# Kernel tuning notes

Hardware: AMD Instinct MI355X
Metric: run time of the kernel (lower is better)

The kernel has to match this reference:

```python
import jax, jax.numpy as jnp
import numpy as np

D_MODEL = 128
NUM_HEADS = 4
D_HEAD = 32
ATTN_COEFF = 0.5
BATCH = 2
SEQ = 4096


def setup_inputs() -> dict:
    key = jax.random.key(0)
    k1, k2, k3, k4, k5 = jax.random.split(key, 5)
    std = 1.0 / np.sqrt(D_MODEL)
    x = jax.random.normal(k1, (BATCH, SEQ, D_MODEL), dtype=jnp.float32)
    W_K = jax.random.normal(k2, (NUM_HEADS, D_HEAD, D_MODEL), dtype=jnp.float32) * std
    W_Q = jax.random.normal(k3, (NUM_HEADS, D_HEAD, D_MODEL), dtype=jnp.float32) * std
    W_V = jax.random.normal(k4, (NUM_HEADS, D_HEAD, D_MODEL), dtype=jnp.float32) * std
    W_O = jax.random.normal(k5, (D_MODEL, NUM_HEADS * D_HEAD), dtype=jnp.float32) * std
    return {"x": x, "W_K": W_K, "W_Q": W_Q, "W_V": W_V, "W_O": W_O}


def reference(x, W_K, W_Q, W_V, W_O):
    batch, seq, _ = x.shape
    # projections: [B, H, S, Dh]
    k = jnp.einsum('ihd,bpd->biph', W_K, x)
    q = jnp.einsum('ihd,bpd->biph', W_Q, x)
    v = jnp.einsum('ihd,bpd->biph', W_V, x)
    # scores: [B, H, Sq, Sk]
    scores = jnp.einsum('biph,biqh->biqp', k, q) / np.sqrt(D_HEAD).astype(np.float32)
    # NOTE: original code builds a causal mask but never applies it; faithful omission.
    attn = jax.nn.softmax(scores, axis=-1)
    # post-softmax affine blend with uniform offset
    attn = attn * ATTN_COEFF + (1.0 - ATTN_COEFF)
    z = jnp.einsum('biph,biqp->biqh', v, attn)          # [B, H, S, Dh]
    z_flat = jnp.transpose(z, (0, 2, 1, 3)).reshape(batch, seq, NUM_HEADS * D_HEAD)
    out = jnp.einsum('df,bpf->bpd', W_O, z_flat)        # [B, S, D]
    return out
```

## Files before the change

### kernel.cpp

```cpp
#include <hip/hip_runtime.h>

#define SQ 4096
#define NB 2
#define NH 4
#define DH 32
#define DM 128

typedef float f32x16 __attribute__((ext_vector_type(16)));
typedef float f32x4  __attribute__((ext_vector_type(4)));
typedef __bf16 bf16x8 __attribute__((ext_vector_type(8)));
typedef unsigned int uint4v __attribute__((ext_vector_type(4)));
typedef unsigned short u16;

#define AS1 __attribute__((address_space(1)))
#define AS3 __attribute__((address_space(3)))

union B8 { uint4v u; bf16x8 b; };

__device__ inline u16 f2bf(float x) {
  unsigned u = __builtin_bit_cast(unsigned, x);
  unsigned r = (u + 0x7FFF + ((u >> 16) & 1)) >> 16;
  return (u16)r;
}

__device__ inline unsigned cvt_pk_bf16(float a, float b) {
  unsigned r;
  asm("v_cvt_pk_bf16_f32 %0, %1, %2" : "=v"(r) : "v"(a), "v"(b));
  return r;
}

__device__ inline void swap32(unsigned &a, unsigned &b) {
  asm("v_permlane32_swap_b32 %0, %1" : "+v"(a), "+v"(b));
}

#if __has_builtin(__builtin_amdgcn_exp2f)
#define EX2 __builtin_amdgcn_exp2f
#else
#define EX2 exp2f
#endif

__device__ inline float xhalf_add(float x) {
  unsigned ua = __builtin_bit_cast(unsigned, x), ub = ua;
  asm("v_permlane32_swap_b32 %0, %1" : "+v"(ua), "+v"(ub));
  return __builtin_bit_cast(float, ua) + __builtin_bit_cast(float, ub);
}

__device__ inline void gload16(const void* g, void* l) {
  __builtin_amdgcn_global_load_lds((const AS1 void*)g, (AS3 void*)l, 16, 0, 0);
}

__device__ inline bf16x8 ld_cvt8(const float* p) {
  f32x4 a = *(const f32x4*)p;
  f32x4 b = *(const f32x4*)(p + 4);
  B8 r;
  r.u[0] = cvt_pk_bf16(a[0], a[1]);
  r.u[1] = cvt_pk_bf16(a[2], a[3]);
  r.u[2] = cvt_pk_bf16(b[0], b[1]);
  r.u[3] = cvt_pk_bf16(b[2], b[3]);
  return r.b;
}

__global__ __launch_bounds__(256) void kprep(const float* __restrict__ x,
                                             const float* __restrict__ Wo,
                                             u16* __restrict__ wob,
                                             float* __restrict__ xsum) {
  const int bid = blockIdx.x, t = threadIdx.x;
  if (bid < 256) {
    const int b = bid >> 7, rblk = bid & 127;
    const int d = t & 127, rh = t >> 7;
    const float* xp = x + ((size_t)b * SQ + rblk * 32) * DM + d;
    float a = 0.f;
    for (int r = rh; r < 32; r += 2) a += xp[(size_t)r * DM];
    __shared__ float red[2][DM];
    red[rh][d] = a;
    __syncthreads();
    if (t < DM) atomicAdd(&xsum[b * DM + t], red[0][t] + red[1][t]);
  } else {
    for (int i = t; i < DM * DM; i += 256) wob[i] = f2bf(Wo[i]);
  }
}

__global__ __launch_bounds__(256) void kprojc(const float* __restrict__ x,
                                              const float* __restrict__ Wk,
                                              const float* __restrict__ Wq,
                                              const float* __restrict__ Wv,
                                              const float* __restrict__ Wo,
                                              const float* __restrict__ xsum,
                                              u16* __restrict__ qb,
                                              u16* __restrict__ kb,
                                              u16* __restrict__ vt,
                                              float* __restrict__ cvec) {
  const int by = blockIdx.y;
  const int t = threadIdx.x;
  if (by == 12) {
    if (blockIdx.x >= NB) return;
    const int b = blockIdx.x;
    __shared__ float xs[DM], vs[DM];
    if (t < DM) xs[t] = xsum[b * DM + t];
    __syncthreads();
    const int c = t >> 1, half = t & 1;
    float a = 0.f;
    const float* wr = Wv + c * DM + half * 64;
    const float* xh = xs + half * 64;
    for (int i = 0; i < 64; ++i) a += wr[i] * xh[i];
    a += __shfl_xor(a, 1, 64);
    if (half == 0) vs[c] = a;
    __syncthreads();
    float a2 = 0.f;
    const float* wr2 = Wo + c * DM + half * 64;
    const float* vh = vs + half * 64;
    for (int i = 0; i < 64; ++i) a2 += wr2[i] * vh[i];
    a2 += __shfl_xor(a2, 1, 64);
    if (half == 0) cvec[b * DM + c] = 0.5f * a2;
    return;
  }
  const int lane = t & 63, wid = t >> 6;
  const int l31 = lane & 31, hi = lane >> 5;
  const int mat = by >> 2, h = by & 3;
  const int p0 = (blockIdx.x * 4 + wid) * 32;
  const float* xrow = x + (size_t)(p0 + l31) * DM + 8 * hi;
  const float* W = (mat == 0) ? Wk : (mat == 1 ? Wq : Wv);
  const float* wrow = W + (h * 32 + l31) * DM + 8 * hi;
  f32x16 acc;
#pragma unroll
  for (int r = 0; r < 16; ++r) acc[r] = 0.f;
#pragma unroll
  for (int ks = 0; ks < 8; ++ks) {
    bf16x8 af = ld_cvt8(xrow + ks * 16);
    bf16x8 wf = ld_cvt8(wrow + ks * 16);
    acc = __builtin_amdgcn_mfma_f32_32x32x16_bf16(af, wf, acc, 0, 0, 0);
  }
  const float QS = 1.4426950408889634f / 5.656854249492380f;
  const int b = p0 >> 12, pl = p0 & (SQ - 1);
  const size_t bh = (size_t)b * NH + h;
  if (mat == 0) {
    u16* dst = kb + (bh * SQ + pl) * DH + l31;
#pragma unroll
    for (int r = 0; r < 16; ++r) {
      int row = (r & 3) + 8 * (r >> 2) + 4 * hi;
      dst[(size_t)row * DH] = f2bf(acc[r]);
    }
  } else if (mat == 1) {
    u16* dst = qb + (bh * SQ + pl) * DH + l31;
#pragma unroll
    for (int r = 0; r < 16; ++r) {
      int row = (r & 3) + 8 * (r >> 2) + 4 * hi;
      dst[(size_t)row * DH] = f2bf(acc[r] * QS);
    }
  } else {
    u16* dst = vt + ((bh * (SQ / 32) + (pl >> 5)) * DH + l31) * 32;
#pragma unroll
    for (int r = 0; r < 16; ++r) {
      int row = (r & 3) + 8 * (r >> 2) + 4 * hi;
      dst[row] = f2bf(acc[r]);
    }
  }
}

#define STAGE(T, B) {                                              \
  const char* kg_ = kgbase + (size_t)(T) * 8192;                   \
  const char* vg_ = vgbase + (size_t)(T) * 8192;                   \
  gload16(kg_,        &klds[B][woff]);                             \
  gload16(kg_ + 1024, &klds[B][woff + 1024]);                      \
  gload16(vg_,        &vlds[B][woff]);                             \
  gload16(vg_ + 1024, &vlds[B][woff + 1024]);                      \
}

#define SUB(S) {                                                                   \
  const int off_ = (S)*2048 + lbase;                                               \
  B8 k0_, k1_;                                                                     \
  k0_.u = *(const uint4v*)(kl + off_ + kx0);                                       \
  k1_.u = *(const uint4v*)(kl + off_ + kx1);                                       \
  __builtin_amdgcn_s_setprio(1);                                                   \
  f32x16 sc = __builtin_amdgcn_mfma_f32_32x32x16_bf16(k0_.b, qf0.b, zacc, 0,0,0);  \
  sc = __builtin_amdgcn_mfma_f32_32x32x16_bf16(k1_.b, qf1.b, sc, 0, 0, 0);         \
  __builtin_amdgcn_s_setprio(0);                                                   \
  float p_[16];                                                                    \
  _Pragma("unroll") for (int r = 0; r < 16; ++r) p_[r] = EX2(sc[r]);               \
  float ls = ((p_[0]+p_[1])+(p_[2]+p_[3]))+((p_[4]+p_[5])+(p_[6]+p_[7]));          \
  ls += ((p_[8]+p_[9])+(p_[10]+p_[11]))+((p_[12]+p_[13])+(p_[14]+p_[15]));         \
  s += ls;                                                                         \
  unsigned w0 = cvt_pk_bf16(p_[0], p_[1]),  w1 = cvt_pk_bf16(p_[2], p_[3]);        \
  unsigned w2 = cvt_pk_bf16(p_[4], p_[5]),  w3 = cvt_pk_bf16(p_[6], p_[7]);        \
  unsigned w4 = cvt_pk_bf16(p_[8], p_[9]),  w5 = cvt_pk_bf16(p_[10], p_[11]);      \
  unsigned w6 = cvt_pk_bf16(p_[12], p_[13]), w7 = cvt_pk_bf16(p_[14], p_[15]);     \
  swap32(w0, w2); swap32(w1, w3); swap32(w4, w6); swap32(w5, w7);                  \
  B8 bp0_, bp1_;                                                                   \
  bp0_.u[0] = w0; bp0_.u[1] = w1; bp0_.u[2] = w2; bp0_.u[3] = w3;                  \
  bp1_.u[0] = w4; bp1_.u[1] = w5; bp1_.u[2] = w6; bp1_.u[3] = w7;                  \
  B8 v0_, v1_;                                                                     \
  v0_.u = *(const uint4v*)(vl + off_ + kx0);                                       \
  v1_.u = *(const uint4v*)(vl + off_ + kx1);                                       \
  __builtin_amdgcn_s_setprio(1);                                                   \
  acc = __builtin_amdgcn_mfma_f32_32x32x16_bf16(v0_.b, bp0_.b, acc, 0, 0, 0);      \
  acc = __builtin_amdgcn_mfma_f32_32x32x16_bf16(v1_.b, bp1_.b, acc, 0, 0, 0);      \
  __builtin_amdgcn_s_setprio(0);                                                   \
}

__global__ __launch_bounds__(256) void kattn(const u16* __restrict__ qb,
                                             const u16* __restrict__ kb,
                                             const u16* __restrict__ vt,
                                             u16* __restrict__ yb) {
  __shared__ char klds[2][8192];
  __shared__ char vlds[2][8192];
  const int t = threadIdx.x, lane = t & 63, wid = t >> 6;
  const int l31 = lane & 31, hi = lane >> 5;
  const int bh = blockIdx.x & 7;
  const int qbase = (blockIdx.x >> 3) * 128 + wid * 32;

  const u16* qrow = qb + ((size_t)bh * SQ + qbase + l31) * DH + 8 * hi;
  B8 qf0, qf1;
  qf0.u = *(const uint4v*)(qrow);
  qf1.u = *(const uint4v*)(qrow + 16);

  const int srcswz = ((lane >> 2) * 64) + ((((lane & 3) ^ ((lane >> 3) & 3))) << 4);
  const int woff = wid * 2048;
  const char* kgbase = (const char*)(kb + (size_t)bh * SQ * DH) + woff + srcswz;
  const char* vgbase = (const char*)(vt + (size_t)bh * (SQ / 32) * DH * 32) + woff + srcswz;

  const int x_ = (l31 >> 1) & 3;
  const int kx0 = (hi ^ x_) << 4;
  const int kx1 = ((2 + hi) ^ x_) << 4;
  const int lbase = l31 * 64;

  f32x16 zacc, acc;
#pragma unroll
  for (int r = 0; r < 16; ++r) { zacc[r] = -16.f; acc[r] = 0.f; }
  float s = 0.f;

  STAGE(0, 0)
  __syncthreads();

  for (int ti = 0; ti < 32; ++ti) {
    const int cur = ti & 1;
    if (ti + 1 < 32) STAGE(ti + 1, cur ^ 1)
    const char* kl = klds[cur];
    const char* vl = vlds[cur];
    SUB(0) SUB(1) SUB(2) SUB(3)
    __syncthreads();
  }

  s = xhalf_add(s);
  float inv = 0.5f / s;
  const int b = bh >> 2, h = bh & 3;
  u16* yp = yb + ((size_t)(b * SQ) + qbase + l31) * DM + h * 32;
#pragma unroll
  for (int r = 0; r < 16; ++r) {
    int row = (r & 3) + 8 * (r >> 2) + 4 * hi;
    yp[row] = f2bf(acc[r] * inv);
  }
}

__global__ __launch_bounds__(256) void kout(const u16* __restrict__ yb,
                                            const u16* __restrict__ wob,
                                            const float* __restrict__ cvec,
                                            float* __restrict__ out) {
  const int t = threadIdx.x, lane = t & 63, wid = t >> 6;
  const int l31 = lane & 31, hi = lane >> 5;
  const int blk = blockIdx.x;
  const int b = blk >> 7;
  const int p0 = (blk & 127) * 32;
  const int d0 = wid * 32;
  const u16* yrow = yb + ((size_t)(b * SQ) + p0 + l31) * DM + 8 * hi;
  const u16* wrow = wob + (size_t)(d0 + l31) * DM + 8 * hi;
  f32x16 acc;
#pragma unroll
  for (int r = 0; r < 16; ++r) acc[r] = 0.f;
#pragma unroll
  for (int ks = 0; ks < 8; ++ks) {
    B8 a, w;
    a.u = *(const uint4v*)(yrow + ks * 16);
    w.u = *(const uint4v*)(wrow + ks * 16);
    acc = __builtin_amdgcn_mfma_f32_32x32x16_bf16(a.b, w.b, acc, 0, 0, 0);
  }
  float cv = cvec[b * DM + d0 + l31];
  float* op = out + ((size_t)(b * SQ) + p0) * DM + d0 + l31;
#pragma unroll
  for (int r = 0; r < 16; ++r) {
    int row = (r & 3) + 8 * (r >> 2) + 4 * hi;
    op[(size_t)row * DM] = acc[r] + cv;
  }
}

extern "C" void kernel_launch(void* const* d_in, const int* in_sizes, int n_in,
                              void* d_out, int out_size, void* d_ws, size_t ws_size,
                              hipStream_t stream) {
  const float* x  = (const float*)d_in[0];
  const float* Wk = (const float*)d_in[1];
  const float* Wq = (const float*)d_in[2];
  const float* Wv = (const float*)d_in[3];
  const float* Wo = (const float*)d_in[4];
  float* out = (float*)d_out;
  char* ws = (char*)d_ws;
  float* xsum = (float*)(ws);
  float* cvec = (float*)(ws + (4 << 10));
  u16* wob = (u16*)(ws + (64 << 10));
  u16* qb = (u16*)(ws + (256 << 10));
  u16* kb = (u16*)(ws + (256 << 10) + ((size_t)2 << 20));
  u16* vt = (u16*)(ws + (256 << 10) + ((size_t)4 << 20));
  u16* yb = (u16*)(ws + (256 << 10) + ((size_t)6 << 20));

  hipMemsetAsync(xsum, 0, NB * DM * sizeof(float), stream);
  kprep<<<dim3(257), dim3(256), 0, stream>>>(x, Wo, wob, xsum);
  kprojc<<<dim3(64, 13), dim3(256), 0, stream>>>(x, Wk, Wq, Wv, Wo, xsum, qb, kb, vt, cvec);
  kattn<<<dim3(256), dim3(256), 0, stream>>>(qb, kb, vt, yb);
  kout<<<dim3(256), dim3(256), 0, stream>>>(yb, wob, cvec, out);
}
```

Measured before the change: 145.5 us.

## Split attention keys across wave pairs and merge partial sums in LDS

The attention kernel now handles 64 queries per block instead of 128, with two wave pairs each covering half of the key range. Partial softmax numerators and denominators are combined through shared memory at the end, and the grid doubles to 512 blocks. The LDS layout also drops the XOR swizzle in favour of a plain lane-contiguous layout. The goal is more blocks to fill the CUs, at the cost of a merge step and lower K/V reuse per block. The unswizzled layout may also bring back LDS bank conflicts.

```diff
diff --git a/kernel.cpp b/kernel.cpp
--- a/kernel.cpp
+++ b/kernel.cpp
@@ -157,20 +157,22 @@
   }
 }
 
-#define STAGE(T, B) {                                              \
-  const char* kg_ = kgbase + (size_t)(T) * 8192;                   \
-  const char* vg_ = vgbase + (size_t)(T) * 8192;                   \
-  gload16(kg_,        &klds[B][woff]);                             \
-  gload16(kg_ + 1024, &klds[B][woff + 1024]);                      \
-  gload16(vg_,        &vlds[B][woff]);                             \
-  gload16(vg_ + 1024, &vlds[B][woff + 1024]);                      \
+#define STAGE(T, B) {                                          \
+  const char* kg_ = kg + (size_t)(T) * 4096;                   \
+  const char* vg_ = vg + (size_t)(T) * 4096;                   \
+  char* kd_ = &klds[kh][B][qg * 2048];                         \
+  char* vd_ = &vlds[kh][B][qg * 2048];                         \
+  gload16(kg_,      kd_);                                      \
+  gload16(kg_ + 32, kd_ + 1024);                               \
+  gload16(vg_,      vd_);                                      \
+  gload16(vg_ + 32, vd_ + 1024);                               \
 }
 
 #define SUB(S) {                                                                   \
-  const int off_ = (S)*2048 + lbase;                                               \
+  const int off_ = (S) * 2048 + lane * 16;                                         \
   B8 k0_, k1_;                                                                     \
-  k0_.u = *(const uint4v*)(kl + off_ + kx0);                                       \
-  k1_.u = *(const uint4v*)(kl + off_ + kx1);                                       \
+  k0_.u = *(const uint4v*)(kl + off_);                                             \
+  k1_.u = *(const uint4v*)(kl + off_ + 1024);                                      \
   __builtin_amdgcn_s_setprio(1);                                                   \
   f32x16 sc = __builtin_amdgcn_mfma_f32_32x32x16_bf16(k0_.b, qf0.b, zacc, 0,0,0);  \
   sc = __builtin_amdgcn_mfma_f32_32x32x16_bf16(k1_.b, qf1.b, sc, 0, 0, 0);         \
@@ -189,8 +191,8 @@
   bp0_.u[0] = w0; bp0_.u[1] = w1; bp0_.u[2] = w2; bp0_.u[3] = w3;                  \
   bp1_.u[0] = w4; bp1_.u[1] = w5; bp1_.u[2] = w6; bp1_.u[3] = w7;                  \
   B8 v0_, v1_;                                                                     \
-  v0_.u = *(const uint4v*)(vl + off_ + kx0);                                       \
-  v1_.u = *(const uint4v*)(vl + off_ + kx1);                                       \
+  v0_.u = *(const uint4v*)(vl + off_);                                             \
+  v1_.u = *(const uint4v*)(vl + off_ + 1024);                                      \
   __builtin_amdgcn_s_setprio(1);                                                   \
   acc = __builtin_amdgcn_mfma_f32_32x32x16_bf16(v0_.b, bp0_.b, acc, 0, 0, 0);      \
   acc = __builtin_amdgcn_mfma_f32_32x32x16_bf16(v1_.b, bp1_.b, acc, 0, 0, 0);      \
@@ -201,27 +203,24 @@
                                              const u16* __restrict__ kb,
                                              const u16* __restrict__ vt,
                                              u16* __restrict__ yb) {
-  __shared__ char klds[2][8192];
-  __shared__ char vlds[2][8192];
+  __shared__ char klds[2][2][4096];
+  __shared__ char vlds[2][2][4096];
+  __shared__ float mrg_s[2][64];
+  __shared__ float mrg_a[2][16][64];
   const int t = threadIdx.x, lane = t & 63, wid = t >> 6;
   const int l31 = lane & 31, hi = lane >> 5;
+  const int qg = wid & 1, kh = wid >> 1;
   const int bh = blockIdx.x & 7;
-  const int qbase = (blockIdx.x >> 3) * 128 + wid * 32;
+  const int qbase = (blockIdx.x >> 3) * 64 + qg * 32;
 
   const u16* qrow = qb + ((size_t)bh * SQ + qbase + l31) * DH + 8 * hi;
   B8 qf0, qf1;
   qf0.u = *(const uint4v*)(qrow);
   qf1.u = *(const uint4v*)(qrow + 16);
 
-  const int srcswz = ((lane >> 2) * 64) + ((((lane & 3) ^ ((lane >> 3) & 3))) << 4);
-  const int woff = wid * 2048;
-  const char* kgbase = (const char*)(kb + (size_t)bh * SQ * DH) + woff + srcswz;
-  const char* vgbase = (const char*)(vt + (size_t)bh * (SQ / 32) * DH * 32) + woff + srcswz;
-
-  const int x_ = (l31 >> 1) & 3;
-  const int kx0 = (hi ^ x_) << 4;
-  const int kx1 = ((2 + hi) ^ x_) << 4;
-  const int lbase = l31 * 64;
+  const int srcoff = (lane & 31) * 64 + (lane >> 5) * 16;
+  const char* kg = (const char*)(kb + (size_t)bh * SQ * DH) + kh * 131072 + qg * 2048 + srcoff;
+  const char* vg = (const char*)(vt + (size_t)bh * SQ * DH) + kh * 131072 + qg * 2048 + srcoff;
 
   f32x16 zacc, acc;
 #pragma unroll
@@ -234,20 +233,30 @@
   for (int ti = 0; ti < 32; ++ti) {
     const int cur = ti & 1;
     if (ti + 1 < 32) STAGE(ti + 1, cur ^ 1)
-    const char* kl = klds[cur];
-    const char* vl = vlds[cur];
-    SUB(0) SUB(1) SUB(2) SUB(3)
+    const char* kl = &klds[kh][cur][0];
+    const char* vl = &vlds[kh][cur][0];
+    SUB(0) SUB(1)
     __syncthreads();
   }
 
   s = xhalf_add(s);
-  float inv = 0.5f / s;
-  const int b = bh >> 2, h = bh & 3;
-  u16* yp = yb + ((size_t)(b * SQ) + qbase + l31) * DM + h * 32;
-#pragma unroll
-  for (int r = 0; r < 16; ++r) {
-    int row = (r & 3) + 8 * (r >> 2) + 4 * hi;
-    yp[row] = f2bf(acc[r] * inv);
+  if (kh == 1) {
+    mrg_s[qg][lane] = s;
+#pragma unroll
+    for (int r = 0; r < 16; ++r) mrg_a[qg][r][lane] = acc[r];
+  }
+  __syncthreads();
+  if (kh == 0) {
+    float den = s + mrg_s[qg][lane];
+    float inv = 0.5f / den;
+    const int b = bh >> 2, h = bh & 3;
+    u16* yp = yb + ((size_t)(b * SQ) + qbase + l31) * DM + h * 32;
+#pragma unroll
+    for (int r = 0; r < 16; ++r) {
+      float o = acc[r] + mrg_a[qg][r][lane];
+      int row = (r & 3) + 8 * (r >> 2) + 4 * hi;
+      yp[row] = f2bf(o * inv);
+    }
   }
 }
 
@@ -303,6 +312,6 @@
   hipMemsetAsync(xsum, 0, NB * DM * sizeof(float), stream);
   kprep<<<dim3(257), dim3(256), 0, stream>>>(x, Wo, wob, xsum);
   kprojc<<<dim3(64, 13), dim3(256), 0, stream>>>(x, Wk, Wq, Wv, Wo, xsum, qb, kb, vt, cvec);
-  kattn<<<dim3(256), dim3(256), 0, stream>>>(qb, kb, vt, yb);
+  kattn<<<dim3(512), dim3(256), 0, stream>>>(qb, kb, vt, yb);
   kout<<<dim3(256), dim3(256), 0, stream>>>(yb, wob, cvec, out);
 }
```

Measured after the change: 133.1 us. -8.6%, faster.
